# Optimization experiments

Measured on AMD Instinct MI355X. Metric: run time of the kernel, lower is better.

## Reference

```python
import jax, jax.numpy as jnp
import numpy as np

B, C, H, W, A = 64, 1280, 7, 7, 40  # batch, in_features, spatial, num_attr


def h_swish(x):
    # x * relu6(x + 3) / 6
    return x * jnp.clip(x + 3.0, 0.0, 6.0) * (1.0 / 6.0)


def setup_inputs() -> dict:
    key = jax.random.key(0)
    kx, k1, k2, k3, k4 = jax.random.split(key, 5)
    s1 = 1.0 / np.sqrt(C)
    return {
        "x": jax.random.normal(kx, (B, C, H, W), dtype=jnp.float32),
        # batched per-attribute head params: Linear(C,C) then Linear(C,1)
        "W1": jax.random.uniform(k1, (A, C, C), jnp.float32, -s1, s1),
        "b1": jax.random.uniform(k2, (A, C), jnp.float32, -s1, s1),
        "W2": jax.random.uniform(k3, (A, C), jnp.float32, -s1, s1),
        "b2": jax.random.uniform(k4, (A,), jnp.float32, -s1, s1),
    }


def reference(x, W1, b1, W2, b2):
    # AdaptiveAvgPool2d((1,1)) + h_swish, then flatten -> [B, C]
    p = h_swish(jnp.mean(x, axis=(2, 3)))
    # all per-attribute heads as one batched GEMM: [B,C] x [A,C,C] -> [B,A,C]
    h = h_swish(jnp.einsum("bc,acd->bad", p, W1) + b1)
    # second layer: Linear(C,1) per attr -> [B, A]
    out = jnp.einsum("bac,ac->ba", h, W2) + b2
    # eval mode (self.training == False): sigmoid applied, dropout inactive
    return jax.nn.sigmoid(out)
```

## Files before the change

### kernel.cpp

```cpp
#include <hip/hip_runtime.h>
#include <hip/hip_bf16.h>

#define B_    64
#define C_    1280
#define HW_   49
#define A_    40
#define BN    128
#define BK    32
#define NK    (C_/BK)
#define NTILE (C_/BN)
#define WLDS_STRIDE 40

typedef short bf16x8 __attribute__((ext_vector_type(8)));
typedef short bf16x4 __attribute__((ext_vector_type(4)));
typedef float f32x4  __attribute__((ext_vector_type(4)));

__device__ __forceinline__ float hswish(float x) {
    float t = fminf(fmaxf(x + 3.0f, 0.0f), 6.0f);
    return x * t * (1.0f / 6.0f);
}

__device__ __forceinline__ short f2bf(float f) {
    __hip_bfloat16 h = __float2bfloat16(f);
    return __builtin_bit_cast(short, h);
}

__global__ __launch_bounds__(256) void pool_kernel(const float* __restrict__ x,
                                                   __hip_bfloat16* __restrict__ p) {
    int t = blockIdx.x * 256 + threadIdx.x;
    const float* src = x + (size_t)t * HW_;
    float s = 0.f;
    #pragma unroll
    for (int i = 0; i < HW_; ++i) s += src[i];
    s *= (1.0f / 49.0f);
    p[t] = __float2bfloat16(hswish(s));
}

__global__ __launch_bounds__(256) void head_kernel(
    const short* __restrict__ p,
    const float* __restrict__ W1,
    const float* __restrict__ b1,
    const float* __restrict__ W2,
    float* __restrict__ part)
{
    __shared__ short w_lds[BN * WLDS_STRIDE];
    __shared__ short p_lds[B_ * BK];

    const int tid  = threadIdx.x;
    const int lane = tid & 63;
    const int wid  = tid >> 6;
    const int ntile = blockIdx.x;
    const int a     = blockIdx.y;
    const int n0    = ntile * BN;

    const int l15 = lane & 15;
    const int lg  = lane >> 4;

    const int sd  = tid & 127;
    const int scg = (tid >> 7) * 16;
    const float* w1base = W1 + (size_t)a * C_ * C_ + n0 + sd;

    const int prow = tid >> 2;
    const int pkof = (tid & 3) * 8;

    f32x4 acc[8];
    #pragma unroll
    for (int n = 0; n < 8; ++n) acc[n] = (f32x4){0.f, 0.f, 0.f, 0.f};

    float  wcur[16];
    bf16x8 pcur;
    {
        #pragma unroll
        for (int i = 0; i < 4; ++i) {
            int cb = scg + i * 4;
            #pragma unroll
            for (int j = 0; j < 4; ++j)
                wcur[i * 4 + j] = w1base[(size_t)(cb + j) * C_];
        }
        pcur = *reinterpret_cast<const bf16x8*>(p + prow * C_ + pkof);
    }

    for (int kt = 0; kt < NK; ++kt) {
        __syncthreads();

        #pragma unroll
        for (int i = 0; i < 4; ++i) {
            int cb = scg + i * 4;
            bf16x4 v;
            v[0] = f2bf(wcur[i * 4 + 0]);
            v[1] = f2bf(wcur[i * 4 + 1]);
            v[2] = f2bf(wcur[i * 4 + 2]);
            v[3] = f2bf(wcur[i * 4 + 3]);
            *reinterpret_cast<bf16x4*>(&w_lds[sd * WLDS_STRIDE + cb]) = v;
        }
        *reinterpret_cast<bf16x8*>(&p_lds[prow * BK + pkof]) = pcur;

        __syncthreads();

        float  wnxt[16];
        bf16x8 pnxt;
        if (kt + 1 < NK) {
            int k0n = (kt + 1) * BK;
            const float* wb = w1base + (size_t)k0n * C_;
            #pragma unroll
            for (int i = 0; i < 4; ++i) {
                int cb = scg + i * 4;
                #pragma unroll
                for (int j = 0; j < 4; ++j)
                    wnxt[i * 4 + j] = wb[(size_t)(cb + j) * C_];
            }
            pnxt = *reinterpret_cast<const bf16x8*>(p + prow * C_ + k0n + pkof);
        }

        bf16x8 afrag = *reinterpret_cast<const bf16x8*>(&p_lds[(wid * 16 + l15) * BK + lg * 8]);
        #pragma unroll
        for (int n = 0; n < 8; ++n) {
            bf16x8 bfrag = *reinterpret_cast<const bf16x8*>(
                &w_lds[(n * 16 + l15) * WLDS_STRIDE + lg * 8]);
            acc[n] = __builtin_amdgcn_mfma_f32_16x16x32_bf16(afrag, bfrag, acc[n], 0, 0, 0);
        }

        #pragma unroll
        for (int i = 0; i < 16; ++i) wcur[i] = wnxt[i];
        pcur = pnxt;
    }

    float partial[4] = {0.f, 0.f, 0.f, 0.f};
    #pragma unroll
    for (int n = 0; n < 8; ++n) {
        int d = n0 + n * 16 + l15;
        float b1v = b1[a * C_ + d];
        float w2v = W2[a * C_ + d];
        #pragma unroll
        for (int r = 0; r < 4; ++r) {
            float h = hswish(acc[n][r] + b1v);
            partial[r] += h * w2v;
        }
    }
    #pragma unroll
    for (int off = 8; off >= 1; off >>= 1) {
        #pragma unroll
        for (int r = 0; r < 4; ++r)
            partial[r] += __shfl_xor(partial[r], off, 64);
    }
    if (l15 == 0) {
        int brow = wid * 16 + lg * 4;
        #pragma unroll
        for (int r = 0; r < 4; ++r)
            part[ntile * (B_ * A_) + (brow + r) * A_ + a] = partial[r];
    }
}

__global__ __launch_bounds__(256) void fin_kernel(const float* __restrict__ part,
                                                  const float* __restrict__ b2,
                                                  float* __restrict__ out) {
    int idx = blockIdx.x * 256 + threadIdx.x;
    if (idx >= B_ * A_) return;
    int a = idx % A_;
    float s = b2[a];
    #pragma unroll
    for (int nb = 0; nb < NTILE; ++nb) s += part[nb * (B_ * A_) + idx];
    out[idx] = 1.0f / (1.0f + expf(-s));
}

extern "C" void kernel_launch(void* const* d_in, const int* in_sizes, int n_in,
                              void* d_out, int out_size, void* d_ws, size_t ws_size,
                              hipStream_t stream) {
    const float* x  = (const float*)d_in[0];
    const float* W1 = (const float*)d_in[1];
    const float* b1 = (const float*)d_in[2];
    const float* W2 = (const float*)d_in[3];
    const float* b2 = (const float*)d_in[4];
    float* out = (float*)d_out;

    __hip_bfloat16* p = (__hip_bfloat16*)d_ws;
    float* part = (float*)((char*)d_ws + (size_t)B_ * C_ * 2);

    pool_kernel<<<(B_ * C_) / 256, 256, 0, stream>>>(x, p);
    head_kernel<<<dim3(NTILE, A_), 256, 0, stream>>>((const short*)p, W1, b1, W2, part);
    fin_kernel<<<(B_ * A_ + 255) / 256, 256, 0, stream>>>(part, b2, out);
}
```

Baseline: 57.22 us.

## Drop LDS staging in head GEMM; load MFMA fragments directly from global

The head kernel now gives each wave its own 32-column slice of the 128-wide tile. Each wave reads W1 and pooled activations straight from global memory into registers in MFMA fragment layout, double-buffered two k-steps ahead. This removes the LDS round trip and two block barriers per k-step, and combines wave results with a small shared reduction at the end. The pool kernel is also changed to stage 64 rows through LDS using coalesced float4 loads instead of strided per-thread reads. The risks are higher register pressure and global W1 reads that are less coalesced, and each wave now reloads the shared activation rows on its own.

```diff
diff --git a/kernel.cpp b/kernel.cpp
--- a/kernel.cpp
+++ b/kernel.cpp
@@ -6,13 +6,10 @@
 #define HW_   49
 #define A_    40
 #define BN    128
-#define BK    32
-#define NK    (C_/BK)
+#define NK    (C_/32)
 #define NTILE (C_/BN)
-#define WLDS_STRIDE 40
 
 typedef short bf16x8 __attribute__((ext_vector_type(8)));
-typedef short bf16x4 __attribute__((ext_vector_type(4)));
 typedef float f32x4  __attribute__((ext_vector_type(4)));
 
 __device__ __forceinline__ float hswish(float x) {
@@ -25,129 +22,137 @@
     return __builtin_bit_cast(short, h);
 }
 
+#define POOL_ROWS 64
 __global__ __launch_bounds__(256) void pool_kernel(const float* __restrict__ x,
                                                    __hip_bfloat16* __restrict__ p) {
-    int t = blockIdx.x * 256 + threadIdx.x;
-    const float* src = x + (size_t)t * HW_;
-    float s = 0.f;
+    __shared__ float buf[POOL_ROWS * HW_];
+    const int tid = threadIdx.x;
+    const size_t base = (size_t)blockIdx.x * (POOL_ROWS * HW_);
+    const float4* src = reinterpret_cast<const float4*>(x + base);
     #pragma unroll
-    for (int i = 0; i < HW_; ++i) s += src[i];
-    s *= (1.0f / 49.0f);
-    p[t] = __float2bfloat16(hswish(s));
+    for (int i = 0; i < 3; ++i) {
+        float4 v = src[tid + i * 256];
+        *reinterpret_cast<float4*>(&buf[(tid + i * 256) * 4]) = v;
+    }
+    if (tid < 16) {
+        float4 v = src[768 + tid];
+        *reinterpret_cast<float4*>(&buf[(768 + tid) * 4]) = v;
+    }
+    __syncthreads();
+    if (tid < POOL_ROWS) {
+        float s = 0.f;
+        #pragma unroll
+        for (int j = 0; j < HW_; ++j) s += buf[tid * HW_ + j];
+        s *= (1.0f / 49.0f);
+        p[blockIdx.x * POOL_ROWS + tid] = __float2bfloat16(hswish(s));
+    }
 }
 
-__global__ __launch_bounds__(256) void head_kernel(
+__global__ __launch_bounds__(256, 4) void head_kernel(
     const short* __restrict__ p,
     const float* __restrict__ W1,
     const float* __restrict__ b1,
     const float* __restrict__ W2,
     float* __restrict__ part)
 {
-    __shared__ short w_lds[BN * WLDS_STRIDE];
-    __shared__ short p_lds[B_ * BK];
+    __shared__ float red[4][B_];
 
     const int tid  = threadIdx.x;
     const int lane = tid & 63;
     const int wid  = tid >> 6;
     const int ntile = blockIdx.x;
     const int a     = blockIdx.y;
-    const int n0    = ntile * BN;
+    const int n0    = ntile * BN + wid * 32;
 
     const int l15 = lane & 15;
     const int lg  = lane >> 4;
 
-    const int sd  = tid & 127;
-    const int scg = (tid >> 7) * 16;
-    const float* w1base = W1 + (size_t)a * C_ * C_ + n0 + sd;
+    const float* bbase = W1 + (size_t)a * C_ * C_ + (size_t)(lg * 8) * C_ + n0 + l15;
+    const short* pbase = p + (size_t)l15 * C_ + lg * 8;
 
-    const int prow = tid >> 2;
-    const int pkof = (tid & 3) * 8;
+    float  braw[2][16];
+    bf16x8 agr[2][4];
+    f32x4  acc[4][2];
+    #pragma unroll
+    for (int m = 0; m < 4; ++m)
+        #pragma unroll
+        for (int n = 0; n < 2; ++n) acc[m][n] = (f32x4){0.f, 0.f, 0.f, 0.f};
 
-    f32x4 acc[8];
+#define LOADB(KT, PH) do {                                          \
+        const float* _b = bbase + (size_t)(KT) * 32 * C_;           \
+        _Pragma("unroll")                                           \
+        for (int j = 0; j < 8; ++j) {                               \
+            braw[PH][j]     = _b[(size_t)j * C_];                   \
+            braw[PH][8 + j] = _b[(size_t)j * C_ + 16];              \
+        }                                                           \
+    } while (0)
+
+#define LOADA(KT, PH) do {                                          \
+        const short* _p = pbase + (KT) * 32;                        \
+        _Pragma("unroll")                                           \
+        for (int m = 0; m < 4; ++m)                                 \
+            agr[PH][m] = *reinterpret_cast<const bf16x8*>(_p + (size_t)m * 16 * C_); \
+    } while (0)
+
+    LOADB(0, 0); LOADA(0, 0);
+    LOADB(1, 1); LOADA(1, 1);
+
     #pragma unroll
-    for (int n = 0; n < 8; ++n) acc[n] = (f32x4){0.f, 0.f, 0.f, 0.f};
+    for (int kt = 0; kt < NK; ++kt) {
+        const int ph = kt & 1;
+        bf16x8 bfrag[2];
+        #pragma unroll
+        for (int n = 0; n < 2; ++n)
+            #pragma unroll
+            for (int j = 0; j < 8; ++j)
+                bfrag[n][j] = f2bf(braw[ph][n * 8 + j]);
+        if (kt + 2 < NK) LOADB(kt + 2, ph);
+        #pragma unroll
+        for (int m = 0; m < 4; ++m)
+            #pragma unroll
+            for (int n = 0; n < 2; ++n)
+                acc[m][n] = __builtin_amdgcn_mfma_f32_16x16x32_bf16(agr[ph][m], bfrag[n], acc[m][n], 0, 0, 0);
+        if (kt + 2 < NK) LOADA(kt + 2, ph);
+    }
+#undef LOADB
+#undef LOADA
 
-    float  wcur[16];
-    bf16x8 pcur;
-    {
-        #pragma unroll
-        for (int i = 0; i < 4; ++i) {
-            int cb = scg + i * 4;
-            #pragma unroll
-            for (int j = 0; j < 4; ++j)
-                wcur[i * 4 + j] = w1base[(size_t)(cb + j) * C_];
-        }
-        pcur = *reinterpret_cast<const bf16x8*>(p + prow * C_ + pkof);
+    float b1v[2], w2v[2];
+    #pragma unroll
+    for (int n = 0; n < 2; ++n) {
+        int col = n0 + n * 16 + l15;
+        b1v[n] = b1[a * C_ + col];
+        w2v[n] = W2[a * C_ + col];
     }
-
-    for (int kt = 0; kt < NK; ++kt) {
-        __syncthreads();
-
-        #pragma unroll
-        for (int i = 0; i < 4; ++i) {
-            int cb = scg + i * 4;
-            bf16x4 v;
-            v[0] = f2bf(wcur[i * 4 + 0]);
-            v[1] = f2bf(wcur[i * 4 + 1]);
-            v[2] = f2bf(wcur[i * 4 + 2]);
-            v[3] = f2bf(wcur[i * 4 + 3]);
-            *reinterpret_cast<bf16x4*>(&w_lds[sd * WLDS_STRIDE + cb]) = v;
-        }
-        *reinterpret_cast<bf16x8*>(&p_lds[prow * BK + pkof]) = pcur;
-
-        __syncthreads();
-
-        float  wnxt[16];
-        bf16x8 pnxt;
-        if (kt + 1 < NK) {
-            int k0n = (kt + 1) * BK;
-            const float* wb = w1base + (size_t)k0n * C_;
-            #pragma unroll
-            for (int i = 0; i < 4; ++i) {
-                int cb = scg + i * 4;
-                #pragma unroll
-                for (int j = 0; j < 4; ++j)
-                    wnxt[i * 4 + j] = wb[(size_t)(cb + j) * C_];
-            }
-            pnxt = *reinterpret_cast<const bf16x8*>(p + prow * C_ + k0n + pkof);
-        }
-
-        bf16x8 afrag = *reinterpret_cast<const bf16x8*>(&p_lds[(wid * 16 + l15) * BK + lg * 8]);
-        #pragma unroll
-        for (int n = 0; n < 8; ++n) {
-            bf16x8 bfrag = *reinterpret_cast<const bf16x8*>(
-                &w_lds[(n * 16 + l15) * WLDS_STRIDE + lg * 8]);
-            acc[n] = __builtin_amdgcn_mfma_f32_16x16x32_bf16(afrag, bfrag, acc[n], 0, 0, 0);
-        }
-
-        #pragma unroll
-        for (int i = 0; i < 16; ++i) wcur[i] = wnxt[i];
-        pcur = pnxt;
-    }
-
-    float partial[4] = {0.f, 0.f, 0.f, 0.f};
+    float partial[4][4];
     #pragma unroll
-    for (int n = 0; n < 8; ++n) {
-        int d = n0 + n * 16 + l15;
-        float b1v = b1[a * C_ + d];
-        float w2v = W2[a * C_ + d];
+    for (int m = 0; m < 4; ++m)
         #pragma unroll
         for (int r = 0; r < 4; ++r) {
-            float h = hswish(acc[n][r] + b1v);
-            partial[r] += h * w2v;
+            float s = 0.f;
+            #pragma unroll
+            for (int n = 0; n < 2; ++n)
+                s += hswish(acc[m][n][r] + b1v[n]) * w2v[n];
+            partial[m][r] = s;
         }
+    #pragma unroll
+    for (int off = 8; off >= 1; off >>= 1)
+        #pragma unroll
+        for (int m = 0; m < 4; ++m)
+            #pragma unroll
+            for (int r = 0; r < 4; ++r)
+                partial[m][r] += __shfl_xor(partial[m][r], off, 64);
+    if (l15 == 0) {
+        #pragma unroll
+        for (int m = 0; m < 4; ++m)
+            #pragma unroll
+            for (int r = 0; r < 4; ++r)
+                red[wid][m * 16 + lg * 4 + r] = partial[m][r];
     }
-    #pragma unroll
-    for (int off = 8; off >= 1; off >>= 1) {
-        #pragma unroll
-        for (int r = 0; r < 4; ++r)
-            partial[r] += __shfl_xor(partial[r], off, 64);
-    }
-    if (l15 == 0) {
-        int brow = wid * 16 + lg * 4;
-        #pragma unroll
-        for (int r = 0; r < 4; ++r)
-            part[ntile * (B_ * A_) + (brow + r) * A_ + a] = partial[r];
+    __syncthreads();
+    if (tid < B_) {
+        float s = red[0][tid] + red[1][tid] + red[2][tid] + red[3][tid];
+        part[ntile * (B_ * A_) + tid * A_ + a] = s;
     }
 }
 
@@ -176,7 +181,7 @@
     __hip_bfloat16* p = (__hip_bfloat16*)d_ws;
     float* part = (float*)((char*)d_ws + (size_t)B_ * C_ * 2);
 
-    pool_kernel<<<(B_ * C_) / 256, 256, 0, stream>>>(x, p);
+    pool_kernel<<<(B_ * C_) / POOL_ROWS, 256, 0, stream>>>(x, p);
     head_kernel<<<dim3(NTILE, A_), 256, 0, stream>>>((const short*)p, W1, b1, W2, part);
     fin_kernel<<<(B_ * A_ + 255) / 256, 256, 0, stream>>>(part, b2, out);
 }
```

Result: slower. 93.24 us (+63.0%).

## Double K tile, swizzle LDS layouts, and coalesce pooling loads via shared memory

Applied to the files above, without the earlier changes.

The head GEMM K tile grows from 32 to 64, so each thread prefetches 32 weight floats per iteration and the K loop has half as many barriers. The padded LDS stride is replaced by an XOR swizzle on the W and p tiles to avoid bank conflicts. The pooling kernel now stages 64 rows into shared memory with float4 coalesced loads before 64 threads reduce them, replacing strided per-thread reads. Register pressure rises from the larger prefetch buffer, and the pool kernel leaves most of its threads idle during the reduction.

```diff
diff --git a/kernel.cpp b/kernel.cpp
--- a/kernel.cpp
+++ b/kernel.cpp
@@ -6,13 +6,11 @@
 #define HW_   49
 #define A_    40
 #define BN    128
-#define BK    32
-#define NK    (C_/BK)
+#define BK    64
+#define NKT   (C_/BK)
 #define NTILE (C_/BN)
-#define WLDS_STRIDE 40
 
 typedef short bf16x8 __attribute__((ext_vector_type(8)));
-typedef short bf16x4 __attribute__((ext_vector_type(4)));
 typedef float f32x4  __attribute__((ext_vector_type(4)));
 
 __device__ __forceinline__ float hswish(float x) {
@@ -25,15 +23,34 @@
     return __builtin_bit_cast(short, h);
 }
 
+__device__ __forceinline__ int swz(int r, int k) {
+    return r * BK + ((((k >> 3) ^ r) & 7) << 3) + (k & 7);
+}
+
+#define POOL_ROWS 64
 __global__ __launch_bounds__(256) void pool_kernel(const float* __restrict__ x,
                                                    __hip_bfloat16* __restrict__ p) {
-    int t = blockIdx.x * 256 + threadIdx.x;
-    const float* src = x + (size_t)t * HW_;
-    float s = 0.f;
+    __shared__ float buf[POOL_ROWS * HW_];
+    const int tid = threadIdx.x;
+    const size_t base = (size_t)blockIdx.x * (POOL_ROWS * HW_);
+    const float4* src = reinterpret_cast<const float4*>(x + base);
     #pragma unroll
-    for (int i = 0; i < HW_; ++i) s += src[i];
-    s *= (1.0f / 49.0f);
-    p[t] = __float2bfloat16(hswish(s));
+    for (int i = 0; i < 3; ++i) {
+        float4 v = src[tid + i * 256];
+        *reinterpret_cast<float4*>(&buf[(tid + i * 256) * 4]) = v;
+    }
+    if (tid < 16) {
+        float4 v = src[768 + tid];
+        *reinterpret_cast<float4*>(&buf[(768 + tid) * 4]) = v;
+    }
+    __syncthreads();
+    if (tid < POOL_ROWS) {
+        float s = 0.f;
+        #pragma unroll
+        for (int j = 0; j < HW_; ++j) s += buf[tid * HW_ + j];
+        s *= (1.0f / 49.0f);
+        p[blockIdx.x * POOL_ROWS + tid] = __float2bfloat16(hswish(s));
+    }
 }
 
 __global__ __launch_bounds__(256) void head_kernel(
@@ -43,7 +60,7 @@
     const float* __restrict__ W2,
     float* __restrict__ part)
 {
-    __shared__ short w_lds[BN * WLDS_STRIDE];
+    __shared__ short w_lds[BN * BK];
     __shared__ short p_lds[B_ * BK];
 
     const int tid  = threadIdx.x;
@@ -56,93 +73,81 @@
     const int l15 = lane & 15;
     const int lg  = lane >> 4;
 
-    const int sd  = tid & 127;
-    const int scg = (tid >> 7) * 16;
+    const int sd = tid & 127;
+    const int kh = (tid >> 7) * 32;
     const float* w1base = W1 + (size_t)a * C_ * C_ + n0 + sd;
 
-    const int prow = tid >> 2;
-    const int pkof = (tid & 3) * 8;
+    const int pr = tid & 63;
+    const int ks = (tid >> 6) * 16;
+    const short* pbase = p + (size_t)pr * C_ + ks;
 
     f32x4 acc[8];
     #pragma unroll
     for (int n = 0; n < 8; ++n) acc[n] = (f32x4){0.f, 0.f, 0.f, 0.f};
 
-    float  wcur[16];
-    bf16x8 pcur;
-    {
+    float  wraw[32];
+    bf16x8 praw[2];
+
+#define LOADW(KT) do {                                              \
+        const float* _wb = w1base + (size_t)((KT) * BK + kh) * C_;  \
+        _Pragma("unroll")                                           \
+        for (int _i = 0; _i < 32; ++_i)                             \
+            wraw[_i] = _wb[(size_t)_i * C_];                        \
+    } while (0)
+
+#define LOADP(KT) do {                                              \
+        const short* _pb = pbase + (KT) * BK;                       \
+        praw[0] = *reinterpret_cast<const bf16x8*>(_pb);            \
+        praw[1] = *reinterpret_cast<const bf16x8*>(_pb + 8);        \
+    } while (0)
+
+    LOADW(0); LOADP(0);
+
+    for (int kt = 0; kt < NKT; ++kt) {
+        __syncthreads();
         #pragma unroll
         for (int i = 0; i < 4; ++i) {
-            int cb = scg + i * 4;
+            bf16x8 v;
             #pragma unroll
-            for (int j = 0; j < 4; ++j)
-                wcur[i * 4 + j] = w1base[(size_t)(cb + j) * C_];
+            for (int j = 0; j < 8; ++j) v[j] = f2bf(wraw[i * 8 + j]);
+            *reinterpret_cast<bf16x8*>(&w_lds[swz(sd, kh + i * 8)]) = v;
         }
-        pcur = *reinterpret_cast<const bf16x8*>(p + prow * C_ + pkof);
-    }
-
-    for (int kt = 0; kt < NK; ++kt) {
+        *reinterpret_cast<bf16x8*>(&p_lds[swz(pr, ks)])     = praw[0];
+        *reinterpret_cast<bf16x8*>(&p_lds[swz(pr, ks + 8)]) = praw[1];
         __syncthreads();
 
-        #pragma unroll
-        for (int i = 0; i < 4; ++i) {
-            int cb = scg + i * 4;
-            bf16x4 v;
-            v[0] = f2bf(wcur[i * 4 + 0]);
-            v[1] = f2bf(wcur[i * 4 + 1]);
-            v[2] = f2bf(wcur[i * 4 + 2]);
-            v[3] = f2bf(wcur[i * 4 + 3]);
-            *reinterpret_cast<bf16x4*>(&w_lds[sd * WLDS_STRIDE + cb]) = v;
-        }
-        *reinterpret_cast<bf16x8*>(&p_lds[prow * BK + pkof]) = pcur;
-
-        __syncthreads();
-
-        float  wnxt[16];
-        bf16x8 pnxt;
-        if (kt + 1 < NK) {
-            int k0n = (kt + 1) * BK;
-            const float* wb = w1base + (size_t)k0n * C_;
-            #pragma unroll
-            for (int i = 0; i < 4; ++i) {
-                int cb = scg + i * 4;
-                #pragma unroll
-                for (int j = 0; j < 4; ++j)
-                    wnxt[i * 4 + j] = wb[(size_t)(cb + j) * C_];
-            }
-            pnxt = *reinterpret_cast<const bf16x8*>(p + prow * C_ + k0n + pkof);
-        }
-
-        bf16x8 afrag = *reinterpret_cast<const bf16x8*>(&p_lds[(wid * 16 + l15) * BK + lg * 8]);
-        #pragma unroll
-        for (int n = 0; n < 8; ++n) {
-            bf16x8 bfrag = *reinterpret_cast<const bf16x8*>(
-                &w_lds[(n * 16 + l15) * WLDS_STRIDE + lg * 8]);
-            acc[n] = __builtin_amdgcn_mfma_f32_16x16x32_bf16(afrag, bfrag, acc[n], 0, 0, 0);
-        }
+        if (kt + 1 < NKT) { LOADW(kt + 1); LOADP(kt + 1); }
 
         #pragma unroll
-        for (int i = 0; i < 16; ++i) wcur[i] = wnxt[i];
-        pcur = pnxt;
+        for (int h = 0; h < 2; ++h) {
+            bf16x8 afrag = *reinterpret_cast<const bf16x8*>(
+                &p_lds[swz(wid * 16 + l15, h * 32 + lg * 8)]);
+            #pragma unroll
+            for (int n = 0; n < 8; ++n) {
+                bf16x8 bfrag = *reinterpret_cast<const bf16x8*>(
+                    &w_lds[swz(n * 16 + l15, h * 32 + lg * 8)]);
+                acc[n] = __builtin_amdgcn_mfma_f32_16x16x32_bf16(afrag, bfrag, acc[n], 0, 0, 0);
+            }
+        }
     }
+#undef LOADW
+#undef LOADP
 
     float partial[4] = {0.f, 0.f, 0.f, 0.f};
     #pragma unroll
     for (int n = 0; n < 8; ++n) {
-        int d = n0 + n * 16 + l15;
-        float b1v = b1[a * C_ + d];
-        float w2v = W2[a * C_ + d];
+        int col = n0 + n * 16 + l15;
+        float b1v = b1[a * C_ + col];
+        float w2v = W2[a * C_ + col];
         #pragma unroll
-        for (int r = 0; r < 4; ++r) {
-            float h = hswish(acc[n][r] + b1v);
-            partial[r] += h * w2v;
-        }
+        for (int r = 0; r < 4; ++r)
+            partial[r] += hswish(acc[n][r] + b1v) * w2v;
     }
     #pragma unroll
-    for (int off = 8; off >= 1; off >>= 1) {
+    for (int off = 8; off >= 1; off >>= 1)
         #pragma unroll
         for (int r = 0; r < 4; ++r)
             partial[r] += __shfl_xor(partial[r], off, 64);
-    }
     if (l15 == 0) {
         int brow = wid * 16 + lg * 4;
         #pragma unroll
@@ -176,7 +181,7 @@
     __hip_bfloat16* p = (__hip_bfloat16*)d_ws;
     float* part = (float*)((char*)d_ws + (size_t)B_ * C_ * 2);
 
-    pool_kernel<<<(B_ * C_) / 256, 256, 0, stream>>>(x, p);
+    pool_kernel<<<(B_ * C_) / POOL_ROWS, 256, 0, stream>>>(x, p);
     head_kernel<<<dim3(NTILE, A_), 256, 0, stream>>>((const short*)p, W1, b1, W2, part);
     fin_kernel<<<(B_ * A_ + 255) / 256, 256, 0, stream>>>(part, b2, out);
 }
```

Result: slower. 59.12 us (+3.3%).

## Fuse pool, head GEMM and finalize into one cooperative kernel with grid syncs

Applied to the files above, without the earlier changes.

Merges the three launches into a single cooperative kernel of 400 blocks, separated by grid-wide barriers. Each block issues its first W1 loads before the barrier so they overlap the pooling phase. Pooling is now staged through LDS with coalesced float4 loads, and the finalize step runs in the first few blocks after a second grid sync. The aim is to remove launch gaps and the uncoalesced strided pooling reads, at the price of two grid syncs and a cooperative launch that needs all 400 blocks resident at once.

```diff
diff --git a/kernel.cpp b/kernel.cpp
--- a/kernel.cpp
+++ b/kernel.cpp
@@ -1,5 +1,8 @@
 #include <hip/hip_runtime.h>
 #include <hip/hip_bf16.h>
+#include <hip/hip_cooperative_groups.h>
+
+namespace cg = cooperative_groups;
 
 #define B_    64
 #define C_    1280
@@ -10,6 +13,9 @@
 #define NK    (C_/BK)
 #define NTILE (C_/BN)
 #define WLDS_STRIDE 40
+#define POOL_RPB 256
+#define NPOOLB ((B_*C_)/POOL_RPB)
+#define NBLOCKS (NTILE*A_)
 
 typedef short bf16x8 __attribute__((ext_vector_type(8)));
 typedef short bf16x4 __attribute__((ext_vector_type(4)));
@@ -25,32 +31,30 @@
     return __builtin_bit_cast(short, h);
 }
 
-__global__ __launch_bounds__(256) void pool_kernel(const float* __restrict__ x,
-                                                   __hip_bfloat16* __restrict__ p) {
-    int t = blockIdx.x * 256 + threadIdx.x;
-    const float* src = x + (size_t)t * HW_;
-    float s = 0.f;
-    #pragma unroll
-    for (int i = 0; i < HW_; ++i) s += src[i];
-    s *= (1.0f / 49.0f);
-    p[t] = __float2bfloat16(hswish(s));
-}
-
-__global__ __launch_bounds__(256) void head_kernel(
-    const short* __restrict__ p,
+union LdsU {
+    float pool[POOL_RPB * HW_];
+    struct { short w[BN * WLDS_STRIDE]; short pl[B_ * BK]; } head;
+};
+
+__global__ __launch_bounds__(256) void fused_kernel(
+    const float* __restrict__ x,
     const float* __restrict__ W1,
     const float* __restrict__ b1,
     const float* __restrict__ W2,
-    float* __restrict__ part)
+    const float* __restrict__ b2,
+    short* __restrict__ p,
+    float* __restrict__ part,
+    float* __restrict__ out)
 {
-    __shared__ short w_lds[BN * WLDS_STRIDE];
-    __shared__ short p_lds[B_ * BK];
+    __shared__ LdsU u;
 
     const int tid  = threadIdx.x;
+    const int bid  = blockIdx.x;
     const int lane = tid & 63;
     const int wid  = tid >> 6;
-    const int ntile = blockIdx.x;
-    const int a     = blockIdx.y;
+
+    const int ntile = bid % NTILE;
+    const int a     = bid / NTILE;
     const int n0    = ntile * BN;
 
     const int l15 = lane & 15;
@@ -63,22 +67,36 @@
     const int prow = tid >> 2;
     const int pkof = (tid & 3) * 8;
 
+    float wcur[16];
+    #pragma unroll
+    for (int i = 0; i < 4; ++i) {
+        int cb = scg + i * 4;
+        #pragma unroll
+        for (int j = 0; j < 4; ++j)
+            wcur[i * 4 + j] = w1base[(size_t)(cb + j) * C_];
+    }
+
+    if (bid < NPOOLB) {
+        const size_t base = (size_t)bid * (POOL_RPB * HW_);
+        const float4* src = reinterpret_cast<const float4*>(x + base);
+        for (int i = tid; i < (POOL_RPB * HW_) / 4; i += 256)
+            *reinterpret_cast<float4*>(&u.pool[i * 4]) = src[i];
+        __syncthreads();
+        float s = 0.f;
+        #pragma unroll
+        for (int j = 0; j < HW_; ++j) s += u.pool[tid * HW_ + j];
+        s *= (1.0f / 49.0f);
+        p[bid * POOL_RPB + tid] = f2bf(hswish(s));
+        __syncthreads();
+    }
+
+    cg::this_grid().sync();
+
     f32x4 acc[8];
     #pragma unroll
     for (int n = 0; n < 8; ++n) acc[n] = (f32x4){0.f, 0.f, 0.f, 0.f};
 
-    float  wcur[16];
-    bf16x8 pcur;
-    {
-        #pragma unroll
-        for (int i = 0; i < 4; ++i) {
-            int cb = scg + i * 4;
-            #pragma unroll
-            for (int j = 0; j < 4; ++j)
-                wcur[i * 4 + j] = w1base[(size_t)(cb + j) * C_];
-        }
-        pcur = *reinterpret_cast<const bf16x8*>(p + prow * C_ + pkof);
-    }
+    bf16x8 pcur = *reinterpret_cast<const bf16x8*>(p + prow * C_ + pkof);
 
     for (int kt = 0; kt < NK; ++kt) {
         __syncthreads();
@@ -91,9 +109,9 @@
             v[1] = f2bf(wcur[i * 4 + 1]);
             v[2] = f2bf(wcur[i * 4 + 2]);
             v[3] = f2bf(wcur[i * 4 + 3]);
-            *reinterpret_cast<bf16x4*>(&w_lds[sd * WLDS_STRIDE + cb]) = v;
-        }
-        *reinterpret_cast<bf16x8*>(&p_lds[prow * BK + pkof]) = pcur;
+            *reinterpret_cast<bf16x4*>(&u.head.w[sd * WLDS_STRIDE + cb]) = v;
+        }
+        *reinterpret_cast<bf16x8*>(&u.head.pl[prow * BK + pkof]) = pcur;
 
         __syncthreads();
 
@@ -112,11 +130,11 @@
             pnxt = *reinterpret_cast<const bf16x8*>(p + prow * C_ + k0n + pkof);
         }
 
-        bf16x8 afrag = *reinterpret_cast<const bf16x8*>(&p_lds[(wid * 16 + l15) * BK + lg * 8]);
+        bf16x8 afrag = *reinterpret_cast<const bf16x8*>(&u.head.pl[(wid * 16 + l15) * BK + lg * 8]);
         #pragma unroll
         for (int n = 0; n < 8; ++n) {
             bf16x8 bfrag = *reinterpret_cast<const bf16x8*>(
-                &w_lds[(n * 16 + l15) * WLDS_STRIDE + lg * 8]);
+                &u.head.w[(n * 16 + l15) * WLDS_STRIDE + lg * 8]);
             acc[n] = __builtin_amdgcn_mfma_f32_16x16x32_bf16(afrag, bfrag, acc[n], 0, 0, 0);
         }
 
@@ -149,18 +167,17 @@
         for (int r = 0; r < 4; ++r)
             part[ntile * (B_ * A_) + (brow + r) * A_ + a] = partial[r];
     }
-}
-
-__global__ __launch_bounds__(256) void fin_kernel(const float* __restrict__ part,
-                                                  const float* __restrict__ b2,
-                                                  float* __restrict__ out) {
-    int idx = blockIdx.x * 256 + threadIdx.x;
-    if (idx >= B_ * A_) return;
-    int a = idx % A_;
-    float s = b2[a];
-    #pragma unroll
-    for (int nb = 0; nb < NTILE; ++nb) s += part[nb * (B_ * A_) + idx];
-    out[idx] = 1.0f / (1.0f + expf(-s));
+
+    cg::this_grid().sync();
+
+    if (bid < (B_ * A_) / 256) {
+        int idx = bid * 256 + tid;
+        int aa = idx % A_;
+        float s = b2[aa];
+        #pragma unroll
+        for (int nb = 0; nb < NTILE; ++nb) s += part[nb * (B_ * A_) + idx];
+        out[idx] = 1.0f / (1.0f + expf(-s));
+    }
 }
 
 extern "C" void kernel_launch(void* const* d_in, const int* in_sizes, int n_in,
@@ -173,10 +190,11 @@
     const float* b2 = (const float*)d_in[4];
     float* out = (float*)d_out;
 
-    __hip_bfloat16* p = (__hip_bfloat16*)d_ws;
+    short* p    = (short*)d_ws;
     float* part = (float*)((char*)d_ws + (size_t)B_ * C_ * 2);
 
-    pool_kernel<<<(B_ * C_) / 256, 256, 0, stream>>>(x, p);
-    head_kernel<<<dim3(NTILE, A_), 256, 0, stream>>>((const short*)p, W1, b1, W2, part);
-    fin_kernel<<<(B_ * A_ + 255) / 256, 256, 0, stream>>>(part, b2, out);
-}
+    void* args[] = { (void*)&x, (void*)&W1, (void*)&b1, (void*)&W2, (void*)&b2,
+                     (void*)&p, (void*)&part, (void*)&out };
+    hipLaunchCooperativeKernel((const void*)fused_kernel,
+                               dim3(NBLOCKS), dim3(256), args, 0, stream);
+}
```

Measured after the change: 175.6 us. +206.9%, slower.
